# Optimization experiments

Hardware: AMD Instinct MI355X
Metric: run time of the kernel (lower is better)

The kernel has to match this reference:

```python
import jax
import jax.numpy as jnp
from jax import lax
import numpy as np

INPUT_SIZE = 2
COND_SIZE = 4
HIDDEN = 128
LATENT = 32
DEC_IN = INPUT_SIZE + LATENT + COND_SIZE + 1  # 39
DT = 0.05


def setup_inputs() -> dict:
    key = jax.random.key(0)
    ks = jax.random.split(key, 9)
    B = 8192
    s = 1.0 / np.sqrt(HIDDEN)  # PyTorch LSTM init scale
    z = jax.random.normal(ks[0], (B, LATENT), jnp.float32)
    condition = jax.random.normal(ks[1], (B, COND_SIZE), jnp.float32)
    start_point = jax.random.normal(ks[2], (B, INPUT_SIZE), jnp.float32)
    W_ih = jax.random.uniform(ks[3], (4 * HIDDEN, DEC_IN), jnp.float32, -s, s)
    W_hh = jax.random.uniform(ks[4], (4 * HIDDEN, HIDDEN), jnp.float32, -s, s)
    b_ih = jax.random.uniform(ks[5], (4 * HIDDEN,), jnp.float32, -s, s)
    b_hh = jax.random.uniform(ks[6], (4 * HIDDEN,), jnp.float32, -s, s)
    W_out = jax.random.uniform(ks[7], (INPUT_SIZE, HIDDEN), jnp.float32, -s, s)
    b_out = jax.random.uniform(ks[8], (INPUT_SIZE,), jnp.float32, -s, s)
    return {
        "z": z, "condition": condition, "start_point": start_point,
        "W_ih": W_ih, "W_hh": W_hh, "b_ih": b_ih, "b_hh": b_hh,
        "W_out": W_out, "b_out": b_out, "seq_len": 2048,
    }


def reference(z, condition, start_point, W_ih, W_hh, b_ih, b_hh, W_out, b_out, seq_len):
    B = z.shape[0]
    dt = jnp.full((B, 1), DT, dtype=z.dtype)  # constant delta_t per step
    # precompute the static part of the per-step input projection: [z, cond, dt]
    # columns of W_ih: [x(2) | z(32) | cond(4) | dt(1)]
    static_in = jnp.concatenate([z, condition, dt], axis=-1)  # [B, 37]
    static_proj = static_in @ W_ih[:, INPUT_SIZE:].T + b_ih + b_hh  # [B, 4H]
    W_ih_x = W_ih[:, :INPUT_SIZE]  # [4H, 2]

    def step(carry, _):
        x_t, h, c = carry
        gates = x_t @ W_ih_x.T + static_proj + h @ W_hh.T  # [B, 4H]
        i, f, g, o = jnp.split(gates, 4, axis=-1)
        i = jax.nn.sigmoid(i)
        f = jax.nn.sigmoid(f)
        g = jnp.tanh(g)
        o = jax.nn.sigmoid(o)
        c = f * c + i * g
        h = o * jnp.tanh(c)
        x_next = h @ W_out.T + b_out  # [B, input_size]
        return (x_next, h, c), x_next

    h0 = jnp.zeros((B, HIDDEN), z.dtype)
    c0 = jnp.zeros((B, HIDDEN), z.dtype)
    _, ys = lax.scan(step, (start_point, h0, c0), None, length=seq_len)
    return jnp.transpose(ys, (1, 0, 2))  # [B, seq_len, input_size]
```

## Files before the change

kernel.cpp:

```cpp
#include <hip/hip_runtime.h>

typedef short bf16x8 __attribute__((ext_vector_type(8)));
typedef float f32x4 __attribute__((ext_vector_type(4)));

#define LOG2E 1.44269504088896340736f

__device__ __forceinline__ unsigned short f2bf(float x) {
    unsigned u = __builtin_bit_cast(unsigned, x);
    return (unsigned short)((u + 0x7fffu + ((u >> 16) & 1u)) >> 16);
}

__global__ __launch_bounds__(512, 2)
void lstm_persist(const float* __restrict__ zP, const float* __restrict__ condP,
                  const float* __restrict__ startP, const float* __restrict__ WihP,
                  const float* __restrict__ WhhP, const float* __restrict__ bihP,
                  const float* __restrict__ bhhP, const float* __restrict__ WoutP,
                  const float* __restrict__ boutP, float* __restrict__ outP)
{
    __shared__ unsigned short hist[2 * 8 * 16 * 128];
    char* const lds = (char*)hist;

    const int tid  = threadIdx.x;
    const int wave = tid >> 6;
    const int lane = tid & 63;
    const int lo   = lane & 15;
    const int gq   = lane >> 4;
    const int r0   = blockIdx.x * 32;
    const int hid0 = wave * 16;

    const float K2 = 2.0f * LOG2E;
    const float ss[4] = { -LOG2E, -LOG2E, 2.0f * LOG2E, -LOG2E };

    float wxs0[4], wxs1[4], bias[4];
    bf16x8 bfrag[4][4];
    #pragma unroll
    for (int s = 0; s < 4; ++s) {
        const int col = s * 128 + hid0 + lo;
        const float wx0 = WihP[col * 39 + 0];
        const float wx1 = WihP[col * 39 + 1];
        wxs0[s] = ss[s] * wx0;
        wxs1[s] = ss[s] * wx1;
        bias[s] = bihP[col] + bhhP[col];
        #pragma unroll
        for (int kt = 0; kt < 4; ++kt) {
            bf16x8 f;
            #pragma unroll
            for (int j = 0; j < 8; ++j) {
                const int k = kt * 32 + gq * 8 + j;
                const float w = WhhP[col * 128 + k]
                              + wx0 * WoutP[k] + wx1 * WoutP[128 + k];
                f[j] = (short)f2bf(ss[s] * w);
            }
            bfrag[s][kt] = f;
        }
    }

    bf16x8 wof[4];
    #pragma unroll
    for (int kt = 0; kt < 4; ++kt) {
        bf16x8 f;
        #pragma unroll
        for (int j = 0; j < 8; ++j) {
            const int k = kt * 32 + gq * 8 + j;
            f[j] = (lo < 2) ? (short)f2bf(WoutP[lo * 128 + k]) : (short)0;
        }
        wof[kt] = f;
    }
    const float bo = (lo < 2) ? boutP[lo] : 0.0f;

    f32x4 spA[4], spB[4];
    #pragma unroll
    for (int s = 0; s < 4; ++s)
        #pragma unroll
        for (int rr = 0; rr < 4; ++rr) { spA[s][rr] = bias[s]; spB[s][rr] = bias[s]; }

    for (int j = 0; j < 32; ++j) {
        float w[4];
        #pragma unroll
        for (int s = 0; s < 4; ++s) w[s] = WihP[(s * 128 + hid0 + lo) * 39 + 2 + j];
        #pragma unroll
        for (int rr = 0; rr < 4; ++rr) {
            const int rowA = r0 + gq * 4 + rr;
            const float sa = zP[rowA * 32 + j];
            const float sb = zP[(rowA + 16) * 32 + j];
            #pragma unroll
            for (int s = 0; s < 4; ++s) { spA[s][rr] += sa * w[s]; spB[s][rr] += sb * w[s]; }
        }
    }
    for (int j = 0; j < 4; ++j) {
        float w[4];
        #pragma unroll
        for (int s = 0; s < 4; ++s) w[s] = WihP[(s * 128 + hid0 + lo) * 39 + 34 + j];
        #pragma unroll
        for (int rr = 0; rr < 4; ++rr) {
            const int rowA = r0 + gq * 4 + rr;
            const float sa = condP[rowA * 4 + j];
            const float sb = condP[(rowA + 16) * 4 + j];
            #pragma unroll
            for (int s = 0; s < 4; ++s) { spA[s][rr] += sa * w[s]; spB[s][rr] += sb * w[s]; }
        }
    }
    #pragma unroll
    for (int s = 0; s < 4; ++s) {
        const float w = 0.05f * WihP[(s * 128 + hid0 + lo) * 39 + 38];
        #pragma unroll
        for (int rr = 0; rr < 4; ++rr) {
            spA[s][rr] = ss[s] * (spA[s][rr] + w);
            spB[s][rr] = ss[s] * (spB[s][rr] + w);
        }
    }

    int wroff[4];
    #pragma unroll
    for (int rr = 0; rr < 4; ++rr) {
        const int row = gq * 4 + rr;
        wroff[rr] = (row * 256 + (hid0 + lo) * 2) ^ ((row & 7) << 4);
    }
    int rdoff[4];
    #pragma unroll
    for (int kt = 0; kt < 4; ++kt)
        rdoff[kt] = (lo * 256 + kt * 64 + gq * 16) ^ ((lo & 7) << 4);

    f32x4 cstA = f32x4{0.f, 0.f, 0.f, 0.f};
    f32x4 cstB = f32x4{0.f, 0.f, 0.f, 0.f};

    auto tail = [&](f32x4 (&acc)[4], f32x4& cst, const int wbyte) {
        float h[4];
        #pragma unroll
        for (int rr = 0; rr < 4; ++rr) {
            const float si = __builtin_amdgcn_rcpf(1.0f + __builtin_amdgcn_exp2f(acc[0][rr]));
            const float sf = __builtin_amdgcn_rcpf(1.0f + __builtin_amdgcn_exp2f(acc[1][rr]));
            const float rg = __builtin_amdgcn_rcpf(1.0f + __builtin_amdgcn_exp2f(acc[2][rr]));
            const float so = __builtin_amdgcn_rcpf(1.0f + __builtin_amdgcn_exp2f(acc[3][rr]));
            const float tg = __builtin_fmaf(rg, -2.0f, 1.0f);
            const float cn = __builtin_fmaf(sf, cst[rr], si * tg);
            cst[rr] = cn;
            const float rc = __builtin_amdgcn_rcpf(1.0f + __builtin_amdgcn_exp2f(cn * K2));
            const float tc = __builtin_fmaf(rc, -2.0f, 1.0f);
            h[rr] = so * tc;
        }
        unsigned p01, p23;
        asm("v_cvt_pk_bf16_f32 %0, %1, %2" : "=v"(p01) : "v"(h[0]), "v"(h[1]));
        asm("v_cvt_pk_bf16_f32 %0, %1, %2" : "=v"(p23) : "v"(h[2]), "v"(h[3]));
        *(unsigned short*)(lds + wbyte + wroff[0]) = (unsigned short)(p01 & 0xffffu);
        *(unsigned short*)(lds + wbyte + wroff[1]) = (unsigned short)(p01 >> 16);
        *(unsigned short*)(lds + wbyte + wroff[2]) = (unsigned short)(p23 & 0xffffu);
        *(unsigned short*)(lds + wbyte + wroff[3]) = (unsigned short)(p23 >> 16);
    };

    {
        f32x4 accA[4], accB[4];
        #pragma unroll
        for (int s = 0; s < 4; ++s) { accA[s] = spA[s]; accB[s] = spB[s]; }
        #pragma unroll
        for (int rr = 0; rr < 4; ++rr) {
            const int rowA = r0 + gq * 4 + rr;
            const float a0 = startP[rowA * 2 + 0];
            const float a1 = startP[rowA * 2 + 1];
            const float b0 = startP[(rowA + 16) * 2 + 0];
            const float b1 = startP[(rowA + 16) * 2 + 1];
            #pragma unroll
            for (int s = 0; s < 4; ++s) {
                accA[s][rr] += a0 * wxs0[s] + a1 * wxs1[s];
                accB[s][rr] += b0 * wxs0[s] + b1 * wxs1[s];
            }
        }
        tail(accA, cstA, 0);
        tail(accB, cstB, 32768);
    }
    #pragma unroll
    for (int s = 0; s < 4; ++s) {
        const float bx = wxs0[s] * boutP[0] + wxs1[s] * boutP[1];
        #pragma unroll
        for (int rr = 0; rr < 4; ++rr) { spA[s][rr] += bx; spB[s][rr] += bx; }
    }
    __syncthreads();

    #pragma unroll 1
    for (int t = 1; t < 2048; ++t) {
        const int rbase = ((t - 1) & 7) * 4096;
        const int wbase = (t & 7) * 4096;

        bf16x8 afA[4];
        #pragma unroll
        for (int kt = 0; kt < 4; ++kt)
            afA[kt] = __builtin_bit_cast(bf16x8, *(const f32x4*)(lds + rbase + rdoff[kt]));
        f32x4 accA[4];
        #pragma unroll
        for (int s = 0; s < 4; ++s) {
            f32x4 a = spA[s];
            #pragma unroll
            for (int kt = 0; kt < 4; ++kt)
                a = __builtin_amdgcn_mfma_f32_16x16x32_bf16(afA[kt], bfrag[s][kt], a, 0, 0, 0);
            accA[s] = a;
        }

        bf16x8 afB[4];
        #pragma unroll
        for (int kt = 0; kt < 4; ++kt)
            afB[kt] = __builtin_bit_cast(bf16x8, *(const f32x4*)(lds + 32768 + rbase + rdoff[kt]));
        f32x4 accB[4];
        #pragma unroll
        for (int s = 0; s < 4; ++s) {
            f32x4 a = spB[s];
            #pragma unroll
            for (int kt = 0; kt < 4; ++kt)
                a = __builtin_amdgcn_mfma_f32_16x16x32_bf16(afB[kt], bfrag[s][kt], a, 0, 0, 0);
            accB[s] = a;
        }

        tail(accA, cstA, wbase);
        tail(accB, cstB, 32768 + wbase);
        __syncthreads();

        if ((t & 7) == 7) {
            f32x4 xa = f32x4{0.f, 0.f, 0.f, 0.f};
            f32x4 xb = f32x4{0.f, 0.f, 0.f, 0.f};
            #pragma unroll
            for (int kt = 0; kt < 4; ++kt) {
                const bf16x8 a = __builtin_bit_cast(bf16x8,
                    *(const f32x4*)(lds + wave * 4096 + rdoff[kt]));
                xa = __builtin_amdgcn_mfma_f32_16x16x32_bf16(a, wof[kt], xa, 0, 0, 0);
                const bf16x8 b = __builtin_bit_cast(bf16x8,
                    *(const f32x4*)(lds + 32768 + wave * 4096 + rdoff[kt]));
                xb = __builtin_amdgcn_mfma_f32_16x16x32_bf16(b, wof[kt], xb, 0, 0, 0);
            }
            const int tg = t - 7 + wave;
            if (lo < 2) {
                #pragma unroll
                for (int rr = 0; rr < 4; ++rr) {
                    const int row = gq * 4 + rr;
                    outP[(size_t)(r0 + row) * 4096 + tg * 2 + lo] = xa[rr] + bo;
                    outP[(size_t)(r0 + 16 + row) * 4096 + tg * 2 + lo] = xb[rr] + bo;
                }
            }
            __syncthreads();
        }
    }
}

extern "C" void kernel_launch(void* const* d_in, const int* in_sizes, int n_in,
                              void* d_out, int out_size, void* d_ws, size_t ws_size,
                              hipStream_t stream) {
    const float* z    = (const float*)d_in[0];
    const float* cond = (const float*)d_in[1];
    const float* strt = (const float*)d_in[2];
    const float* Wih  = (const float*)d_in[3];
    const float* Whh  = (const float*)d_in[4];
    const float* bih  = (const float*)d_in[5];
    const float* bhh  = (const float*)d_in[6];
    const float* Wout = (const float*)d_in[7];
    const float* bout = (const float*)d_in[8];
    float* out = (float*)d_out;

    hipLaunchKernelGGL(lstm_persist, dim3(256), dim3(512), 0, stream,
                       z, cond, strt, Wih, Whh, bih, bhh, Wout, bout, out);
}
```

Measured before the change: 2.903 ms.

## Skew the two row-group recurrences and overlap output projection with compute

Offsets the B row-group's LSTM step by half an iteration, so B's tail (transcendentals plus LDS writes) runs between A's MFMAs and B's MFMAs, with a barrier between the halves. This lets matrix and vector work of the two independent sequences interleave. The h history ring grows from 8 to 16 slots, which doubles shared memory to 128KB per block and may limit occupancy to one block per CU instead of two. The extra per-8-step barrier is removed by folding the output projection into the regular step barrier, at the cost of a second barrier on every step.

```diff
diff --git a/kernel.cpp b/kernel.cpp
--- a/kernel.cpp
+++ b/kernel.cpp
@@ -17,7 +17,7 @@
                   const float* __restrict__ bhhP, const float* __restrict__ WoutP,
                   const float* __restrict__ boutP, float* __restrict__ outP)
 {
-    __shared__ unsigned short hist[2 * 8 * 16 * 128];
+    __shared__ unsigned short hist[2 * 16 * 16 * 128];
     char* const lds = (char*)hist;
 
     const int tid  = threadIdx.x;
@@ -123,6 +123,7 @@
 
     f32x4 cstA = f32x4{0.f, 0.f, 0.f, 0.f};
     f32x4 cstB = f32x4{0.f, 0.f, 0.f, 0.f};
+    f32x4 accA[4], accB[4];
 
     auto tail = [&](f32x4 (&acc)[4], f32x4& cst, const int wbyte) {
         float h[4];
@@ -148,10 +149,34 @@
         *(unsigned short*)(lds + wbyte + wroff[3]) = (unsigned short)(p23 >> 16);
     };
 
+    auto outg = [&](const int tb) {
+        const int sbase = ((tb & 15) + wave) * 4096;
+        f32x4 xa = f32x4{0.f, 0.f, 0.f, 0.f};
+        f32x4 xb = f32x4{0.f, 0.f, 0.f, 0.f};
+        #pragma unroll
+        for (int kt = 0; kt < 4; ++kt) {
+            const bf16x8 a = __builtin_bit_cast(bf16x8,
+                *(const f32x4*)(lds + sbase + rdoff[kt]));
+            xa = __builtin_amdgcn_mfma_f32_16x16x32_bf16(a, wof[kt], xa, 0, 0, 0);
+            const bf16x8 b = __builtin_bit_cast(bf16x8,
+                *(const f32x4*)(lds + 65536 + sbase + rdoff[kt]));
+            xb = __builtin_amdgcn_mfma_f32_16x16x32_bf16(b, wof[kt], xb, 0, 0, 0);
+        }
+        const int tg = tb + wave;
+        if (lo < 2) {
+            #pragma unroll
+            for (int rr = 0; rr < 4; ++rr) {
+                const int row = gq * 4 + rr;
+                outP[(size_t)(r0 + row) * 4096 + tg * 2 + lo] = xa[rr] + bo;
+                outP[(size_t)(r0 + 16 + row) * 4096 + tg * 2 + lo] = xb[rr] + bo;
+            }
+        }
+    };
+
     {
-        f32x4 accA[4], accB[4];
-        #pragma unroll
-        for (int s = 0; s < 4; ++s) { accA[s] = spA[s]; accB[s] = spB[s]; }
+        f32x4 accA0[4];
+        #pragma unroll
+        for (int s = 0; s < 4; ++s) { accA0[s] = spA[s]; accB[s] = spB[s]; }
         #pragma unroll
         for (int rr = 0; rr < 4; ++rr) {
             const int rowA = r0 + gq * 4 + rr;
@@ -161,12 +186,11 @@
             const float b1 = startP[(rowA + 16) * 2 + 1];
             #pragma unroll
             for (int s = 0; s < 4; ++s) {
-                accA[s][rr] += a0 * wxs0[s] + a1 * wxs1[s];
-                accB[s][rr] += b0 * wxs0[s] + b1 * wxs1[s];
+                accA0[s][rr] += a0 * wxs0[s] + a1 * wxs1[s];
+                accB[s][rr]  += b0 * wxs0[s] + b1 * wxs1[s];
             }
         }
-        tail(accA, cstA, 0);
-        tail(accB, cstB, 32768);
+        tail(accA0, cstA, 0);
     }
     #pragma unroll
     for (int s = 0; s < 4; ++s) {
@@ -178,14 +202,12 @@
 
     #pragma unroll 1
     for (int t = 1; t < 2048; ++t) {
-        const int rbase = ((t - 1) & 7) * 4096;
-        const int wbase = (t & 7) * 4096;
+        const int rb = ((t - 1) & 15) * 4096;
 
         bf16x8 afA[4];
         #pragma unroll
         for (int kt = 0; kt < 4; ++kt)
-            afA[kt] = __builtin_bit_cast(bf16x8, *(const f32x4*)(lds + rbase + rdoff[kt]));
-        f32x4 accA[4];
+            afA[kt] = __builtin_bit_cast(bf16x8, *(const f32x4*)(lds + rb + rdoff[kt]));
         #pragma unroll
         for (int s = 0; s < 4; ++s) {
             f32x4 a = spA[s];
@@ -194,12 +216,13 @@
                 a = __builtin_amdgcn_mfma_f32_16x16x32_bf16(afA[kt], bfrag[s][kt], a, 0, 0, 0);
             accA[s] = a;
         }
+        tail(accB, cstB, 65536 + rb);
+        __syncthreads();
 
         bf16x8 afB[4];
         #pragma unroll
         for (int kt = 0; kt < 4; ++kt)
-            afB[kt] = __builtin_bit_cast(bf16x8, *(const f32x4*)(lds + 32768 + rbase + rdoff[kt]));
-        f32x4 accB[4];
+            afB[kt] = __builtin_bit_cast(bf16x8, *(const f32x4*)(lds + 65536 + rb + rdoff[kt]));
         #pragma unroll
         for (int s = 0; s < 4; ++s) {
             f32x4 a = spB[s];
@@ -208,35 +231,14 @@
                 a = __builtin_amdgcn_mfma_f32_16x16x32_bf16(afB[kt], bfrag[s][kt], a, 0, 0, 0);
             accB[s] = a;
         }
-
-        tail(accA, cstA, wbase);
-        tail(accB, cstB, 32768 + wbase);
+        tail(accA, cstA, (t & 15) * 4096);
+        if ((t & 7) == 0) outg(t - 8);
         __syncthreads();
-
-        if ((t & 7) == 7) {
-            f32x4 xa = f32x4{0.f, 0.f, 0.f, 0.f};
-            f32x4 xb = f32x4{0.f, 0.f, 0.f, 0.f};
-            #pragma unroll
-            for (int kt = 0; kt < 4; ++kt) {
-                const bf16x8 a = __builtin_bit_cast(bf16x8,
-                    *(const f32x4*)(lds + wave * 4096 + rdoff[kt]));
-                xa = __builtin_amdgcn_mfma_f32_16x16x32_bf16(a, wof[kt], xa, 0, 0, 0);
-                const bf16x8 b = __builtin_bit_cast(bf16x8,
-                    *(const f32x4*)(lds + 32768 + wave * 4096 + rdoff[kt]));
-                xb = __builtin_amdgcn_mfma_f32_16x16x32_bf16(b, wof[kt], xb, 0, 0, 0);
-            }
-            const int tg = t - 7 + wave;
-            if (lo < 2) {
-                #pragma unroll
-                for (int rr = 0; rr < 4; ++rr) {
-                    const int row = gq * 4 + rr;
-                    outP[(size_t)(r0 + row) * 4096 + tg * 2 + lo] = xa[rr] + bo;
-                    outP[(size_t)(r0 + 16 + row) * 4096 + tg * 2 + lo] = xb[rr] + bo;
-                }
-            }
-            __syncthreads();
-        }
-    }
+    }
+
+    tail(accB, cstB, 65536 + 15 * 4096);
+    __syncthreads();
+    outg(2040);
 }
 
 extern "C" void kernel_launch(void* const* d_in, const int* in_sizes, int n_in,
```

New measurement: 2.852 ms (median of 2 runs). Within noise of the previous version (-1.8%).
